# Performance work log

Measured on AMD Instinct MI355X. Metric: run time of the kernel, lower is better.

Reference implementation:

```python
import jax, jax.numpy as jnp
import numpy as np

ATT = 128  # attention_size
D = 128    # entity_embedding_dim


def setup_inputs() -> dict:
    key = jax.random.key(0)
    k1, k2, k3, k4, k5 = jax.random.split(key, 5)
    B, N, K = 1024, 50, 5
    entity_embedding = jax.random.normal(k1, (B, N, D), dtype=jnp.float32)
    neigh_entity_embedding = jax.random.normal(k2, (B, N, K, D), dtype=jnp.float32)
    neigh_relation_embedding = jax.random.normal(k3, (B, N, K, D), dtype=jnp.float32)
    # fc1: Linear(3*D -> ATT), fc2: Linear(ATT -> 1)
    lim1 = 1.0 / np.sqrt(3 * D)
    lim2 = 1.0 / np.sqrt(ATT)
    W1 = jax.random.uniform(k4, (3 * D, ATT), minval=-lim1, maxval=lim1, dtype=jnp.float32)
    b1 = jnp.zeros((ATT,), dtype=jnp.float32)
    W2 = jax.random.uniform(k5, (ATT, 1), minval=-lim2, maxval=lim2, dtype=jnp.float32)
    b2 = jnp.zeros((1,), dtype=jnp.float32)
    return {
        "entity_embedding": entity_embedding,
        "neigh_entity_embedding": neigh_entity_embedding,
        "neigh_relation_embedding": neigh_relation_embedding,
        "W1": W1, "b1": b1, "W2": W2, "b2": b2,
    }


def reference(entity_embedding, neigh_entity_embedding, neigh_relation_embedding, W1, b1, W2, b2):
    B, N, K, Dd = neigh_entity_embedding.shape
    # expand entity to each of the K neighbors: [B, N, K, D]
    ent_exp = jnp.broadcast_to(entity_embedding[:, :, None, :], (B, N, K, Dd))
    # concat along feature dim -> [B, N, K, 3D]
    concat = jnp.concatenate([ent_exp, neigh_entity_embedding, neigh_relation_embedding], axis=3)
    # tiny MLP: fc1 -> fc2 gives one logit per neighbor
    h = jnp.einsum('bnkf,fa->bnka', concat, W1) + b1          # [B, N, K, ATT]
    logits = jnp.einsum('bnka,ao->bnko', h, W2) + b2          # [B, N, K, 1]
    att = jax.nn.softmax(logits, axis=2)                      # softmax over K neighbors
    neigh_att = jnp.sum(att * neigh_entity_embedding, axis=2) # [B, N, D]
    # squeeze() on [B,N,D] with no singleton dims is identity
    return jnp.concatenate([entity_embedding, neigh_att], axis=-1)  # [B, N, 2D]
```

## Files before the change

kernel.cpp:

```cpp
#include <hip/hip_runtime.h>
#include <math.h>


#define DIM 128
#define KN 5

typedef float nfloat4 __attribute__((ext_vector_type(4)));

__device__ __forceinline__ float dot4(nfloat4 a, nfloat4 b) {
    return a.x * b.x + a.y * b.y + a.z * b.z + a.w * b.w;
}

__global__ __launch_bounds__(256) void kgat_prep(
    const float* __restrict__ W1,
    const float* __restrict__ b1,
    const float* __restrict__ W2,
    const float* __restrict__ b2,
    float* __restrict__ ws)
{
    const int gw = blockIdx.x * 4 + (threadIdx.x >> 6);
    const int lane = threadIdx.x & 63;
    if (gw < 3 * DIM) {
        const int t = gw;
        const float2 w1 = *(const float2*)(W1 + (size_t)t * DIM + 2 * lane);
        const float2 w2 = *(const float2*)(W2 + 2 * lane);
        float v = w1.x * w2.x + w1.y * w2.y;
        #pragma unroll
        for (int off = 32; off >= 1; off >>= 1) v += __shfl_xor(v, off, 64);
        if (lane == 0) ws[t] = v;
    } else if (gw == 3 * DIM) {
        const float2 bb = *(const float2*)(b1 + 2 * lane);
        const float2 w2 = *(const float2*)(W2 + 2 * lane);
        float v = bb.x * w2.x + bb.y * w2.y;
        #pragma unroll
        for (int off = 32; off >= 1; off >>= 1) v += __shfl_xor(v, off, 64);
        if (lane == 0) ws[3 * DIM] = v + b2[0];
    }
}

__global__ __launch_bounds__(256) void kgat_main(
    const float* __restrict__ ent,
    const float* __restrict__ ne,
    const float* __restrict__ nr,
    const float* __restrict__ ws,
    float* __restrict__ out,
    int P)
{
    const int wave = threadIdx.x >> 6;
    const int lane = threadIdx.x & 63;
    const int half = lane >> 5;
    const int l    = lane & 31;
    const int p = blockIdx.x * 8 + wave * 2 + half;
    if (p >= P) return;

    const int d = l * 4;
    const nfloat4 we  = *(const nfloat4*)(ws + d);
    const nfloat4 wne = *(const nfloat4*)(ws + DIM + d);
    const nfloat4 wnr = *(const nfloat4*)(ws + 2 * DIM + d);
    const float   c   = ws[3 * DIM];

    const nfloat4 e4 = *(const nfloat4*)(ent + (size_t)p * DIM + d);
    const size_t rowK = ((size_t)p * KN) * DIM + d;
    nfloat4 ne4[KN], nr4[KN];
    #pragma unroll
    for (int k = 0; k < KN; ++k) {
        ne4[k] = *(const nfloat4*)(ne + rowK + (size_t)k * DIM);
        nr4[k] = *(const nfloat4*)(nr + rowK + (size_t)k * DIM);
    }

    float red[KN + 1];
    red[0] = dot4(e4, we);
    #pragma unroll
    for (int k = 0; k < KN; ++k)
        red[k + 1] = dot4(ne4[k], wne) + dot4(nr4[k], wnr);

    #pragma unroll
    for (int j = 0; j < KN + 1; ++j) {
        float v = red[j];
        #pragma unroll
        for (int off = 16; off >= 1; off >>= 1) v += __shfl_xor(v, off, 64);
        red[j] = v;
    }

    float logit[KN];
    float m = -INFINITY;
    #pragma unroll
    for (int k = 0; k < KN; ++k) {
        logit[k] = red[k + 1] + red[0] + c;
        m = fmaxf(m, logit[k]);
    }
    float ex[KN], s = 0.f;
    #pragma unroll
    for (int k = 0; k < KN; ++k) { ex[k] = __expf(logit[k] - m); s += ex[k]; }
    const float inv = 1.f / s;

    nfloat4 acc = {0.f, 0.f, 0.f, 0.f};
    #pragma unroll
    for (int k = 0; k < KN; ++k) {
        const float a = ex[k] * inv;
        acc.x += a * ne4[k].x;
        acc.y += a * ne4[k].y;
        acc.z += a * ne4[k].z;
        acc.w += a * ne4[k].w;
    }

    float* orow = out + (size_t)p * (2 * DIM);
    __builtin_nontemporal_store(e4,  (nfloat4*)(orow + d));
    __builtin_nontemporal_store(acc, (nfloat4*)(orow + DIM + d));
}

extern "C" void kernel_launch(void* const* d_in, const int* in_sizes, int n_in,
                              void* d_out, int out_size, void* d_ws, size_t ws_size,
                              hipStream_t stream) {
    const float* ent = (const float*)d_in[0];
    const float* ne  = (const float*)d_in[1];
    const float* nr  = (const float*)d_in[2];
    const float* W1  = (const float*)d_in[3];
    const float* b1  = (const float*)d_in[4];
    const float* W2  = (const float*)d_in[5];
    const float* b2  = (const float*)d_in[6];
    float* out = (float*)d_out;
    float* ws  = (float*)d_ws;

    const int P = in_sizes[0] / DIM;

    kgat_prep<<<(3 * DIM + 1 + 3) / 4, 256, 0, stream>>>(W1, b1, W2, b2, ws);
    kgat_main<<<(P + 7) / 8, 256, 0, stream>>>(ent, ne, nr, ws, out, P);
}
```

Measured before the change: 313.8 us.

## Make main kernel persistent with grid-stride loop and register double-buffered prefetch

The main kernel now runs a capped grid of at most 1024 blocks. Each half-wave loops over rows with a grid stride and loads the next row's entity, neighbor and relation vectors into a second register set while the current row's reductions, softmax and stores run. The aim is to hide global-load latency and cut the cost of launching and retiring many small blocks. It also drops the constant bias term from the logits, which softmax ignores anyway. In exchange, register pressure roughly doubles and fewer waves are resident to hide latency.

```diff
diff --git a/kernel.cpp b/kernel.cpp
--- a/kernel.cpp
+++ b/kernel.cpp
@@ -38,75 +38,93 @@
     }
 }
 
-__global__ __launch_bounds__(256) void kgat_main(
+__global__ __launch_bounds__(256, 4) void kgat_main(
     const float* __restrict__ ent,
     const float* __restrict__ ne,
     const float* __restrict__ nr,
     const float* __restrict__ ws,
     float* __restrict__ out,
-    int P)
+    int P, int stride)
 {
     const int wave = threadIdx.x >> 6;
     const int lane = threadIdx.x & 63;
     const int half = lane >> 5;
     const int l    = lane & 31;
-    const int p = blockIdx.x * 8 + wave * 2 + half;
+    const int d    = l * 4;
+
+    int p = blockIdx.x * 8 + wave * 2 + half;
     if (p >= P) return;
 
-    const int d = l * 4;
     const nfloat4 we  = *(const nfloat4*)(ws + d);
     const nfloat4 wne = *(const nfloat4*)(ws + DIM + d);
     const nfloat4 wnr = *(const nfloat4*)(ws + 2 * DIM + d);
-    const float   c   = ws[3 * DIM];
 
-    const nfloat4 e4 = *(const nfloat4*)(ent + (size_t)p * DIM + d);
-    const size_t rowK = ((size_t)p * KN) * DIM + d;
-    nfloat4 ne4[KN], nr4[KN];
-    #pragma unroll
-    for (int k = 0; k < KN; ++k) {
-        ne4[k] = *(const nfloat4*)(ne + rowK + (size_t)k * DIM);
-        nr4[k] = *(const nfloat4*)(nr + rowK + (size_t)k * DIM);
+    nfloat4 eA, neA[KN], nrA[KN];
+    nfloat4 eB, neB[KN], nrB[KN];
+
+    auto load_row = [&](int pp, nfloat4& e4, nfloat4 (&n4)[KN], nfloat4 (&r4)[KN]) {
+        e4 = *(const nfloat4*)(ent + (size_t)pp * DIM + d);
+        const size_t rowK = (size_t)pp * (KN * DIM) + d;
+        #pragma unroll
+        for (int k = 0; k < KN; ++k) {
+            n4[k] = *(const nfloat4*)(ne + rowK + (size_t)k * DIM);
+            r4[k] = *(const nfloat4*)(nr + rowK + (size_t)k * DIM);
+        }
+    };
+
+    auto process = [&](int pc, int pn,
+                       nfloat4& e4, nfloat4 (&n4)[KN], nfloat4 (&r4)[KN],
+                       nfloat4& en, nfloat4 (&nn)[KN], nfloat4 (&rn)[KN]) {
+        float red[KN];
+        const float ec = dot4(e4, we);
+        #pragma unroll
+        for (int k = 0; k < KN; ++k)
+            red[k] = ec + dot4(n4[k], wne) + dot4(r4[k], wnr);
+
+        if (pn < P) load_row(pn, en, nn, rn);
+
+        #pragma unroll
+        for (int j = 0; j < KN; ++j) {
+            float v = red[j];
+            #pragma unroll
+            for (int off = 16; off >= 1; off >>= 1) v += __shfl_xor(v, off, 64);
+            red[j] = v;
+        }
+
+        float m = red[0];
+        #pragma unroll
+        for (int k = 1; k < KN; ++k) m = fmaxf(m, red[k]);
+        float ex[KN], s = 0.f;
+        #pragma unroll
+        for (int k = 0; k < KN; ++k) { ex[k] = __expf(red[k] - m); s += ex[k]; }
+        const float inv = 1.f / s;
+
+        nfloat4 acc = {0.f, 0.f, 0.f, 0.f};
+        #pragma unroll
+        for (int k = 0; k < KN; ++k) {
+            const float a = ex[k] * inv;
+            acc.x += a * n4[k].x;
+            acc.y += a * n4[k].y;
+            acc.z += a * n4[k].z;
+            acc.w += a * n4[k].w;
+        }
+
+        float* orow = out + (size_t)pc * (2 * DIM);
+        __builtin_nontemporal_store(e4,  (nfloat4*)(orow + d));
+        __builtin_nontemporal_store(acc, (nfloat4*)(orow + DIM + d));
+    };
+
+    load_row(p, eA, neA, nrA);
+    for (;;) {
+        int pn = p + stride;
+        process(p, pn, eA, neA, nrA, eB, neB, nrB);
+        p = pn;
+        if (p >= P) break;
+        pn = p + stride;
+        process(p, pn, eB, neB, nrB, eA, neA, nrA);
+        p = pn;
+        if (p >= P) break;
     }
-
-    float red[KN + 1];
-    red[0] = dot4(e4, we);
-    #pragma unroll
-    for (int k = 0; k < KN; ++k)
-        red[k + 1] = dot4(ne4[k], wne) + dot4(nr4[k], wnr);
-
-    #pragma unroll
-    for (int j = 0; j < KN + 1; ++j) {
-        float v = red[j];
-        #pragma unroll
-        for (int off = 16; off >= 1; off >>= 1) v += __shfl_xor(v, off, 64);
-        red[j] = v;
-    }
-
-    float logit[KN];
-    float m = -INFINITY;
-    #pragma unroll
-    for (int k = 0; k < KN; ++k) {
-        logit[k] = red[k + 1] + red[0] + c;
-        m = fmaxf(m, logit[k]);
-    }
-    float ex[KN], s = 0.f;
-    #pragma unroll
-    for (int k = 0; k < KN; ++k) { ex[k] = __expf(logit[k] - m); s += ex[k]; }
-    const float inv = 1.f / s;
-
-    nfloat4 acc = {0.f, 0.f, 0.f, 0.f};
-    #pragma unroll
-    for (int k = 0; k < KN; ++k) {
-        const float a = ex[k] * inv;
-        acc.x += a * ne4[k].x;
-        acc.y += a * ne4[k].y;
-        acc.z += a * ne4[k].z;
-        acc.w += a * ne4[k].w;
-    }
-
-    float* orow = out + (size_t)p * (2 * DIM);
-    __builtin_nontemporal_store(e4,  (nfloat4*)(orow + d));
-    __builtin_nontemporal_store(acc, (nfloat4*)(orow + DIM + d));
 }
 
 extern "C" void kernel_launch(void* const* d_in, const int* in_sizes, int n_in,
@@ -125,5 +143,9 @@
     const int P = in_sizes[0] / DIM;
 
     kgat_prep<<<(3 * DIM + 1 + 3) / 4, 256, 0, stream>>>(W1, b1, W2, b2, ws);
-    kgat_main<<<(P + 7) / 8, 256, 0, stream>>>(ent, ne, nr, ws, out, P);
+
+    int nb = (P + 7) / 8;
+    if (nb > 1024) nb = 1024;
+    if (nb < 1) nb = 1;
+    kgat_main<<<nb, 256, 0, stream>>>(ent, ne, nr, ws, out, P, nb * 8);
 }
```

After: 322.9 us. +2.9%, slower.

## Loop rows per half-wave with double-buffered register prefetch

Applied to the files above, without the earlier changes.

The main kernel now launches far fewer blocks. Each half-wave walks several rows, loading the next row's entity, neighbour and relation vectors into a second register buffer while the current row is reduced, put through softmax and stored. Scheduling barriers stop the compiler from reordering the prefetch and the compute. The constant logit bias is dropped because softmax ignores a shared shift, and the entity term is folded in before the shuffle reduction, which removes one reduction chain. The aim is to keep more memory requests in flight per wave and to cut per-block launch overhead. In exchange the block count drops to under four per CU, and the doubled register buffers may lower occupancy.

```diff
diff --git a/kernel.cpp b/kernel.cpp
--- a/kernel.cpp
+++ b/kernel.cpp
@@ -38,75 +38,99 @@
     }
 }
 
-__global__ __launch_bounds__(256) void kgat_main(
+#define LOAD_ROW(pp, e4, n4, r4)                                            \
+    do {                                                                    \
+        e4 = *(const nfloat4*)(ent + (size_t)(pp) * DIM + d);               \
+        const size_t rowK_ = (size_t)(pp) * (KN * DIM) + d;                 \
+        _Pragma("unroll")                                                   \
+        for (int k = 0; k < KN; ++k) {                                      \
+            n4[k] = *(const nfloat4*)(ne + rowK_ + (size_t)k * DIM);        \
+            r4[k] = *(const nfloat4*)(nr + rowK_ + (size_t)k * DIM);        \
+        }                                                                   \
+    } while (0)
+
+#define PROCESS_ROW(pc, e4, n4, r4)                                         \
+    do {                                                                    \
+        float red[KN];                                                      \
+        const float ec = dot4(e4, we);                                      \
+        _Pragma("unroll")                                                   \
+        for (int k = 0; k < KN; ++k)                                        \
+            red[k] = ec + dot4(n4[k], wne) + dot4(r4[k], wnr);              \
+        _Pragma("unroll")                                                   \
+        for (int j = 0; j < KN; ++j) {                                      \
+            float v = red[j];                                               \
+            _Pragma("unroll")                                               \
+            for (int off = 16; off >= 1; off >>= 1)                         \
+                v += __shfl_xor(v, off, 64);                                \
+            red[j] = v;                                                     \
+        }                                                                   \
+        float m = red[0];                                                   \
+        _Pragma("unroll")                                                   \
+        for (int k = 1; k < KN; ++k) m = fmaxf(m, red[k]);                  \
+        float ex[KN], s = 0.f;                                              \
+        _Pragma("unroll")                                                   \
+        for (int k = 0; k < KN; ++k) { ex[k] = __expf(red[k] - m); s += ex[k]; } \
+        const float inv = 1.f / s;                                          \
+        nfloat4 acc = {0.f, 0.f, 0.f, 0.f};                                 \
+        _Pragma("unroll")                                                   \
+        for (int k = 0; k < KN; ++k) {                                      \
+            const float a = ex[k] * inv;                                    \
+            acc.x += a * n4[k].x;                                           \
+            acc.y += a * n4[k].y;                                           \
+            acc.z += a * n4[k].z;                                           \
+            acc.w += a * n4[k].w;                                           \
+        }                                                                   \
+        float* orow_ = out + (size_t)(pc) * (2 * DIM);                      \
+        __builtin_nontemporal_store(e4,  (nfloat4*)(orow_ + d));            \
+        __builtin_nontemporal_store(acc, (nfloat4*)(orow_ + DIM + d));      \
+    } while (0)
+
+__global__ __launch_bounds__(256, 4) void kgat_main(
     const float* __restrict__ ent,
     const float* __restrict__ ne,
     const float* __restrict__ nr,
     const float* __restrict__ ws,
     float* __restrict__ out,
-    int P)
+    int P, int L)
 {
     const int wave = threadIdx.x >> 6;
     const int lane = threadIdx.x & 63;
     const int half = lane >> 5;
     const int l    = lane & 31;
-    const int p = blockIdx.x * 8 + wave * 2 + half;
-    if (p >= P) return;
+    const int d    = l * 4;
+    const int h    = wave * 2 + half;
 
-    const int d = l * 4;
+    const int base = blockIdx.x * (8 * L);
+    int pend = base + 8 * L;
+    if (pend > P) pend = P;
+    int p = base + h;
+    if (p >= pend) return;
+
     const nfloat4 we  = *(const nfloat4*)(ws + d);
     const nfloat4 wne = *(const nfloat4*)(ws + DIM + d);
     const nfloat4 wnr = *(const nfloat4*)(ws + 2 * DIM + d);
-    const float   c   = ws[3 * DIM];
 
-    const nfloat4 e4 = *(const nfloat4*)(ent + (size_t)p * DIM + d);
-    const size_t rowK = ((size_t)p * KN) * DIM + d;
-    nfloat4 ne4[KN], nr4[KN];
-    #pragma unroll
-    for (int k = 0; k < KN; ++k) {
-        ne4[k] = *(const nfloat4*)(ne + rowK + (size_t)k * DIM);
-        nr4[k] = *(const nfloat4*)(nr + rowK + (size_t)k * DIM);
+    nfloat4 eA, neA[KN], nrA[KN];
+    nfloat4 eB, neB[KN], nrB[KN];
+
+    LOAD_ROW(p, eA, neA, nrA);
+    int pn = p + 8;
+
+    for (;;) {
+        if (pn < pend) LOAD_ROW(pn, eB, neB, nrB);
+        __builtin_amdgcn_sched_barrier(0);
+        PROCESS_ROW(p, eA, neA, nrA);
+        p = pn;
+        if (p >= pend) break;
+        pn = p + 8;
+
+        if (pn < pend) LOAD_ROW(pn, eA, neA, nrA);
+        __builtin_amdgcn_sched_barrier(0);
+        PROCESS_ROW(p, eB, neB, nrB);
+        p = pn;
+        if (p >= pend) break;
+        pn = p + 8;
     }
-
-    float red[KN + 1];
-    red[0] = dot4(e4, we);
-    #pragma unroll
-    for (int k = 0; k < KN; ++k)
-        red[k + 1] = dot4(ne4[k], wne) + dot4(nr4[k], wnr);
-
-    #pragma unroll
-    for (int j = 0; j < KN + 1; ++j) {
-        float v = red[j];
-        #pragma unroll
-        for (int off = 16; off >= 1; off >>= 1) v += __shfl_xor(v, off, 64);
-        red[j] = v;
-    }
-
-    float logit[KN];
-    float m = -INFINITY;
-    #pragma unroll
-    for (int k = 0; k < KN; ++k) {
-        logit[k] = red[k + 1] + red[0] + c;
-        m = fmaxf(m, logit[k]);
-    }
-    float ex[KN], s = 0.f;
-    #pragma unroll
-    for (int k = 0; k < KN; ++k) { ex[k] = __expf(logit[k] - m); s += ex[k]; }
-    const float inv = 1.f / s;
-
-    nfloat4 acc = {0.f, 0.f, 0.f, 0.f};
-    #pragma unroll
-    for (int k = 0; k < KN; ++k) {
-        const float a = ex[k] * inv;
-        acc.x += a * ne4[k].x;
-        acc.y += a * ne4[k].y;
-        acc.z += a * ne4[k].z;
-        acc.w += a * ne4[k].w;
-    }
-
-    float* orow = out + (size_t)p * (2 * DIM);
-    __builtin_nontemporal_store(e4,  (nfloat4*)(orow + d));
-    __builtin_nontemporal_store(acc, (nfloat4*)(orow + DIM + d));
 }
 
 extern "C" void kernel_launch(void* const* d_in, const int* in_sizes, int n_in,
@@ -125,5 +149,10 @@
     const int P = in_sizes[0] / DIM;
 
     kgat_prep<<<(3 * DIM + 1 + 3) / 4, 256, 0, stream>>>(W1, b1, W2, b2, ws);
-    kgat_main<<<(P + 7) / 8, 256, 0, stream>>>(ent, ne, nr, ws, out, P);
+
+    int L = (P + 8 * 1024 - 1) / (8 * 1024);
+    if (L < 1) L = 1;
+    int nb = (P + 8 * L - 1) / (8 * L);
+    if (nb < 1) nb = 1;
+    kgat_main<<<nb, 256, 0, stream>>>(ent, ne, nr, ws, out, P, L);
 }
```

New measurement: 330.3 us. 1.05x slower.
